# Optimization experiments

Measured on AMD Instinct MI355X. Metric: run time of the kernel, lower is better.

## Reference

```python
import jax, jax.numpy as jnp
import numpy as np

N_GROUPS = 2048  # (d+1)//2 with d=4096


def setup_inputs() -> dict:
    key = jax.random.key(0)
    k1, k2, k3 = jax.random.split(key, 3)
    x = jax.random.normal(k1, (4096, 4096), dtype=jnp.float32)
    # Lloyd-Max style scalar codebook: sorted 16 levels (2^bits, bits=4)
    centroids = jnp.sort(jax.random.normal(k2, (16,), dtype=jnp.float32))
    # random planar rotations: angles ~ U[0, 2pi), stored as (cos, sin)
    angles = jax.random.uniform(k3, (N_GROUPS,), dtype=jnp.float32) * (2.0 * np.pi)
    rot2 = jnp.stack([jnp.cos(angles), jnp.sin(angles)], axis=-1)
    return {"x": x, "centroids": centroids, "rot2": rot2}


def reference(x, centroids, rot2):
    B, d = x.shape
    n_groups = rot2.shape[0]
    # --- quantize ---
    norms = jnp.clip(jnp.linalg.norm(x, axis=-1, keepdims=True), 1e-8)  # [B,1]
    x_unit = x / norms
    v = x_unit.reshape(B, n_groups, 2)
    c, s = rot2[:, 0], rot2[:, 1]  # [G]
    r0 = c * v[..., 0] - s * v[..., 1]
    r1 = s * v[..., 0] + c * v[..., 1]
    flat = jnp.stack([r0, r1], axis=-1).reshape(B, d)  # rotated coords [B,d]
    # per-scalar nearest-centroid search over n_levels
    indices = jnp.argmin(jnp.abs(flat[..., None] - centroids), axis=-1)  # [B,d]
    # --- dequantize ---
    q = centroids[indices].reshape(B, n_groups, 2)
    f0 = c * q[..., 0] + s * q[..., 1]   # inverse rotation
    f1 = -s * q[..., 0] + c * q[..., 1]
    x_hat = jnp.stack([f0, f1], axis=-1).reshape(B, d) * norms
    return x_hat, indices
```

## Files before the change

kernel.cpp:

```cpp
#include <hip/hip_runtime.h>


#define ROW_D     4096
#define BLOCK_T   256
#define F4_PER_T  4

typedef float f32x4 __attribute__((ext_vector_type(4)));

struct QP { float o0, o1, i0, i1; };

__device__ __forceinline__ QP quant_pair(
    float x0, float x1, float c, float s,
    float invf, float dnf, double invd,
    const float* __restrict__ mf,
    const float4* __restrict__ w4,
    const float* __restrict__ cent)
{
    const float v0 = x0 * invf, v1 = x1 * invf;
    const float r0 = c * v0 - s * v1;
    const float r1 = s * v0 + c * v1;

    int a = 0, b = 0;
#pragma unroll
    for (int j = 0; j < 15; ++j) {
        a += (r0 > mf[j]) ? 1 : 0;
        b += (r1 > mf[j]) ? 1 : 0;
    }

    const float4 pa = w4[a];
    const float4 pb = w4[b];
    float q0 = pa.y, q1 = pb.y;

    const float EPS = 1e-5f;
    const float g0 = fminf(r0 - pa.x, pa.z - r0);
    const float g1 = fminf(r1 - pb.x, pb.z - r1);
    if (g0 < EPS || g1 < EPS) {
        const double v0d = (double)x0 * invd;
        const double v1d = (double)x1 * invd;
        const double cd = (double)c, sd = (double)s;
        const double r0d = cd * v0d - sd * v1d;
        const double r1d = sd * v0d + cd * v1d;
        a = 0; b = 0;
        double q0d = (double)cent[0], q1d = (double)cent[0];
#pragma unroll
        for (int j = 0; j < 15; ++j) {
            const double mj = 0.5 * ((double)cent[j] + (double)cent[j + 1]);
            const bool ca = r0d > mj;
            const bool cb = r1d > mj;
            a += ca ? 1 : 0;
            b += cb ? 1 : 0;
            q0d = ca ? (double)cent[j + 1] : q0d;
            q1d = cb ? (double)cent[j + 1] : q1d;
        }
        q0 = (float)q0d;
        q1 = (float)q1d;
    }

    QP r;
    r.o0 = (c * q0 + s * q1) * dnf;
    r.o1 = (c * q1 - s * q0) * dnf;
    r.i0 = (float)a;
    r.i1 = (float)b;
    return r;
}

__global__ __launch_bounds__(BLOCK_T) void planar_quant_kernel(
    const float* __restrict__ x,
    const float* __restrict__ cent,
    const float* __restrict__ rot2,
    float* __restrict__ out_xhat,
    float* __restrict__ out_idx)
{
    const int row = blockIdx.x;
    const int t   = threadIdx.x;

    const f32x4* xr = (const f32x4*)(x + (size_t)row * ROW_D);
    const float4* rr = (const float4*)rot2;

    __shared__ f32x4  xs[ROW_D / 4];
    __shared__ double smem[5];
    __shared__ float4 w4[16];

    double ss = 0.0;
#pragma unroll
    for (int i = 0; i < F4_PER_T; ++i) {
        f32x4 v = __builtin_nontemporal_load(&xr[t + BLOCK_T * i]);
        xs[t + BLOCK_T * i] = v;
        ss += (double)v.x * (double)v.x;
        ss += (double)v.y * (double)v.y;
        ss += (double)v.z * (double)v.z;
        ss += (double)v.w * (double)v.w;
    }

#pragma unroll
    for (int off = 32; off > 0; off >>= 1)
        ss += __shfl_down(ss, off, 64);

    const int wid = t >> 6;
    if ((t & 63) == 0) smem[wid] = ss;

    float cf[16];
#pragma unroll
    for (int j = 0; j < 16; ++j) cf[j] = cent[j];
    float mf[15];
#pragma unroll
    for (int j = 0; j < 15; ++j) mf[j] = 0.5f * (cf[j] + cf[j + 1]);

    if (t < 16) {
        const float lo = (t == 0)  ? -3.0e38f : 0.5f * (cf[t - 1] + cf[t]);
        const float hi = (t == 15) ?  3.0e38f : 0.5f * (cf[t] + cf[t + 1]);
        w4[t] = make_float4(lo, cf[t], hi, 0.0f);
    }
    __syncthreads();
    if (t == 0) {
        double tot = smem[0] + smem[1] + smem[2] + smem[3];
        double n = sqrt(tot);
        smem[4] = (n < 1e-8) ? 1e-8 : n;
    }
    __syncthreads();
    const double dnd  = smem[4];
    const double invd = 1.0 / dnd;
    const float  dnf  = (float)dnd;
    const float  invf = (float)invd;

    f32x4* xo = (f32x4*)(out_xhat + (size_t)row * ROW_D);
    f32x4* io = (f32x4*)(out_idx  + (size_t)row * ROW_D);

#pragma unroll
    for (int i = 0; i < F4_PER_T; ++i) {
        const int f = t + BLOCK_T * i;
        const f32x4 xv = xs[f];
        const float4 rv = rr[f];
        const QP lo = quant_pair(xv.x, xv.y, rv.x, rv.y, invf, dnf, invd, mf, w4, cent);
        const QP hi = quant_pair(xv.z, xv.w, rv.z, rv.w, invf, dnf, invd, mf, w4, cent);
        f32x4 ov, iv;
        ov.x = lo.o0; ov.y = lo.o1; ov.z = hi.o0; ov.w = hi.o1;
        iv.x = lo.i0; iv.y = lo.i1; iv.z = hi.i0; iv.w = hi.i1;
        __builtin_nontemporal_store(ov, &xo[f]);
        __builtin_nontemporal_store(iv, &io[f]);
    }
}

extern "C" void kernel_launch(void* const* d_in, const int* in_sizes, int n_in,
                              void* d_out, int out_size, void* d_ws, size_t ws_size,
                              hipStream_t stream) {
    const float* x    = (const float*)d_in[0];
    const float* cent = (const float*)d_in[1];
    const float* rot2 = (const float*)d_in[2];

    const int d = in_sizes[2];
    const int B = in_sizes[0] / d;

    float* out  = (float*)d_out;
    float* xhat = out;
    float* idxo = out + (size_t)B * d;

    planar_quant_kernel<<<B, BLOCK_T, 0, stream>>>(x, cent, rot2, xhat, idxo);
}
```

Before: 183.5 us.

## Split fused quantizer into separate row-norm and quantize kernels

Splits the single fused kernel in two. The first kernel computes per-row norms into the workspace, and the second kernel re-reads x from global memory to quantize. This removes the 16KB LDS staging buffer and one barrier from the quantize kernel, which could raise occupancy. In exchange, x (64MB) is read twice and there is an extra kernel launch. The design seems to rely on the second read hitting in cache.

```diff
diff --git a/kernel.cpp b/kernel.cpp
--- a/kernel.cpp
+++ b/kernel.cpp
@@ -64,28 +64,18 @@
     return r;
 }
 
-__global__ __launch_bounds__(BLOCK_T) void planar_quant_kernel(
+__global__ __launch_bounds__(BLOCK_T) void norm_kernel(
     const float* __restrict__ x,
-    const float* __restrict__ cent,
-    const float* __restrict__ rot2,
-    float* __restrict__ out_xhat,
-    float* __restrict__ out_idx)
+    double* __restrict__ norms)
 {
     const int row = blockIdx.x;
     const int t   = threadIdx.x;
-
     const f32x4* xr = (const f32x4*)(x + (size_t)row * ROW_D);
-    const float4* rr = (const float4*)rot2;
-
-    __shared__ f32x4  xs[ROW_D / 4];
-    __shared__ double smem[5];
-    __shared__ float4 w4[16];
 
     double ss = 0.0;
 #pragma unroll
     for (int i = 0; i < F4_PER_T; ++i) {
-        f32x4 v = __builtin_nontemporal_load(&xr[t + BLOCK_T * i]);
-        xs[t + BLOCK_T * i] = v;
+        const f32x4 v = xr[t + BLOCK_T * i];
         ss += (double)v.x * (double)v.x;
         ss += (double)v.y * (double)v.y;
         ss += (double)v.z * (double)v.z;
@@ -96,8 +86,29 @@
     for (int off = 32; off > 0; off >>= 1)
         ss += __shfl_down(ss, off, 64);
 
-    const int wid = t >> 6;
-    if ((t & 63) == 0) smem[wid] = ss;
+    __shared__ double smem[4];
+    if ((t & 63) == 0) smem[t >> 6] = ss;
+    __syncthreads();
+    if (t == 0) {
+        const double tot = smem[0] + smem[1] + smem[2] + smem[3];
+        const double n = sqrt(tot);
+        norms[row] = (n < 1e-8) ? 1e-8 : n;
+    }
+}
+
+__global__ __launch_bounds__(BLOCK_T) void quant_kernel(
+    const float* __restrict__ x,
+    const float* __restrict__ cent,
+    const float* __restrict__ rot2,
+    const double* __restrict__ norms,
+    float* __restrict__ out_xhat,
+    float* __restrict__ out_idx)
+{
+    const int row = blockIdx.x;
+    const int t   = threadIdx.x;
+
+    const f32x4* xr = (const f32x4*)(x + (size_t)row * ROW_D);
+    const float4* rr = (const float4*)rot2;
 
     float cf[16];
 #pragma unroll
@@ -106,22 +117,18 @@
 #pragma unroll
     for (int j = 0; j < 15; ++j) mf[j] = 0.5f * (cf[j] + cf[j + 1]);
 
+    __shared__ float4 w4[16];
     if (t < 16) {
         const float lo = (t == 0)  ? -3.0e38f : 0.5f * (cf[t - 1] + cf[t]);
         const float hi = (t == 15) ?  3.0e38f : 0.5f * (cf[t] + cf[t + 1]);
         w4[t] = make_float4(lo, cf[t], hi, 0.0f);
     }
-    __syncthreads();
-    if (t == 0) {
-        double tot = smem[0] + smem[1] + smem[2] + smem[3];
-        double n = sqrt(tot);
-        smem[4] = (n < 1e-8) ? 1e-8 : n;
-    }
-    __syncthreads();
-    const double dnd  = smem[4];
+
+    const double dnd  = norms[row];
     const double invd = 1.0 / dnd;
     const float  dnf  = (float)dnd;
     const float  invf = (float)invd;
+    __syncthreads();
 
     f32x4* xo = (f32x4*)(out_xhat + (size_t)row * ROW_D);
     f32x4* io = (f32x4*)(out_idx  + (size_t)row * ROW_D);
@@ -129,7 +136,7 @@
 #pragma unroll
     for (int i = 0; i < F4_PER_T; ++i) {
         const int f = t + BLOCK_T * i;
-        const f32x4 xv = xs[f];
+        const f32x4 xv = xr[f];
         const float4 rv = rr[f];
         const QP lo = quant_pair(xv.x, xv.y, rv.x, rv.y, invf, dnf, invd, mf, w4, cent);
         const QP hi = quant_pair(xv.z, xv.w, rv.z, rv.w, invf, dnf, invd, mf, w4, cent);
@@ -155,5 +162,8 @@
     float* xhat = out;
     float* idxo = out + (size_t)B * d;
 
-    planar_quant_kernel<<<B, BLOCK_T, 0, stream>>>(x, cent, rot2, xhat, idxo);
+    double* norms = (double*)d_ws;
+
+    norm_kernel<<<B, BLOCK_T, 0, stream>>>(x, norms);
+    quant_kernel<<<B, BLOCK_T, 0, stream>>>(x, cent, rot2, norms, xhat, idxo);
 }
```

After: 193.1 us. 5.2% more time.
